# Kernel optimization log

Measured on AMD Instinct MI355X. Metric: run time of the kernel, lower is better.

The kernel has to match this reference:

```python
import jax, jax.numpy as jnp
import numpy as np

# static sizes
B, N_PER, D, H, L, DFF, IN_DIM = 32, 1024, 128, 4, 3, 2048, 64
N = B * N_PER
HD = D // H
EPS = 1e-5


def setup_inputs() -> dict:
    key = jax.random.key(0)
    ks = jax.random.split(key, 16)
    s = 0.02
    rn = lambda k, shp: jax.random.normal(k, shp, jnp.float32) * s
    return {
        "x": jax.random.normal(ks[0], (N, IN_DIM), jnp.float32),
        # uniform graph sizes -> static max_nodes; sorted graph ids
        "batch": jnp.repeat(jnp.arange(B, dtype=jnp.int32), N_PER),
        "W_in": rn(ks[1], (D, IN_DIM)),
        "b_in": rn(ks[2], (D,)),
        "Wqkv": rn(ks[3], (L, 3 * D, D)),
        "bqkv": rn(ks[4], (L, 3 * D)),
        "Wo": rn(ks[5], (L, D, D)),
        "bo": rn(ks[6], (L, D)),
        "W1": rn(ks[7], (L, DFF, D)),
        "b1": rn(ks[8], (L, DFF)),
        "W2": rn(ks[9], (L, D, DFF)),
        "b2": rn(ks[10], (L, D)),
        "ln1_g": jnp.ones((L, D), jnp.float32),
        "ln1_b": jnp.zeros((L, D), jnp.float32),
        "ln2_g": jnp.ones((L, D), jnp.float32),
        "ln2_b": jnp.zeros((L, D), jnp.float32),
    }


def _ln(x, g, b):
    m = x.mean(-1, keepdims=True)
    v = jnp.mean((x - m) ** 2, axis=-1, keepdims=True)
    return (x - m) / jnp.sqrt(v + EPS) * g + b


def _mha(h, Wqkv, bqkv, Wo, bo):
    # h: [B, S, D]
    qkv = h @ Wqkv.T + bqkv                      # [B, S, 3D]
    q, k, v = jnp.split(qkv, 3, axis=-1)
    q = q.reshape(B, -1, H, HD)
    k = k.reshape(B, -1, H, HD)
    v = v.reshape(B, -1, H, HD)
    att = jnp.einsum("bqhd,bkhd->bhqk", q, k) / np.sqrt(HD).astype(np.float32)
    p = jax.nn.softmax(att, axis=-1)
    o = jnp.einsum("bhqk,bkhd->bqhd", p, v).reshape(B, -1, D)
    return o @ Wo.T + bo


def reference(x, batch, W_in, b_in, Wqkv, bqkv, Wo, bo, W1, b1, W2, b2,
              ln1_g, ln1_b, ln2_g, ln2_b):
    # fused ragged -> padded: project all nodes once, scatter by (graph, pos)
    h = x @ W_in.T + b_in                        # [N, D]
    starts = jnp.searchsorted(batch, jnp.arange(B, dtype=batch.dtype))
    pos = jnp.arange(N, dtype=batch.dtype) - starts[batch]
    padded = jnp.zeros((B, N_PER, D), h.dtype).at[batch, pos].set(h)

    out = padded
    for l in range(L):  # post-LN TransformerEncoderLayer, dropout=eval
        a = _mha(out, Wqkv[l], bqkv[l], Wo[l], bo[l])
        out = _ln(out + a, ln1_g[l], ln1_b[l])
        f = jax.nn.relu(out @ W1[l].T + b1[l]) @ W2[l].T + b2[l]
        out = _ln(out + f, ln2_g[l], ln2_b[l])

    # mask derived from projected inputs, exactly as the original
    mask = (padded.sum(axis=2) != 0).astype(out.dtype)  # [B, S]
    return (out * mask[:, :, None]).sum(axis=1) / mask.sum(axis=1, keepdims=True)
```

## Files before the change

kernel.cpp:

```cpp
#include <hip/hip_runtime.h>
#include <hip/hip_bf16.h>
#include <stdint.h>

#define BB    32
#define NPER  1024
#define NTOT  32768
#define DD    128
#define HH    4
#define HD    32
#define LL    3
#define DFF   2048
#define INDIM 64
#define QKSCALE 0.17677669529663687f

typedef unsigned short u16;
typedef short bf16x8 __attribute__((ext_vector_type(8)));
typedef float f32x4 __attribute__((ext_vector_type(4)));

#define AS_GLOBAL(p) ((const __attribute__((address_space(1))) void*)(p))
#define AS_LDS(p)    ((__attribute__((address_space(3))) void*)(p))

__device__ __forceinline__ float bf2f(u16 v){
  unsigned u = ((unsigned)v) << 16; float f; __builtin_memcpy(&f, &u, 4); return f;
}
__device__ __forceinline__ u16 f2bf(float f){
  unsigned u; __builtin_memcpy(&u, &f, 4);
  unsigned lsb = (u >> 16) & 1u;
  u += 0x7fffu + lsb;
  return (u16)(u >> 16);
}

constexpr size_t OFF_FLAG   = 0;
constexpr size_t OFF_STARTS = 256;
constexpr size_t OFF_BIN    = 1024;
constexpr size_t OFF_BQKV   = OFF_BIN   + 128*4;
constexpr size_t OFF_BO     = OFF_BQKV  + 1152*4;
constexpr size_t OFF_B1     = OFF_BO    + 384*4;
constexpr size_t OFF_B2     = OFF_B1    + 6144*4;
constexpr size_t OFF_LN1G   = OFF_B2    + 384*4;
constexpr size_t OFF_LN1B   = OFF_LN1G  + 384*4;
constexpr size_t OFF_LN2G   = OFF_LN1B  + 384*4;
constexpr size_t OFF_LN2B   = OFF_LN2G  + 384*4;
constexpr size_t OFF_XB     = 40960;
constexpr size_t OFF_WINB   = OFF_XB    + (size_t)2097152*2;
constexpr size_t OFF_WQKVB  = OFF_WINB  + (size_t)8192*2;
constexpr size_t OFF_WOB    = OFF_WQKVB + (size_t)147456*2;
constexpr size_t OFF_W1B    = OFF_WOB   + (size_t)49152*2;
constexpr size_t OFF_W2B    = OFF_W1B   + (size_t)786432*2;
constexpr size_t OFF_CUR    = OFF_W2B   + (size_t)786432*2;
constexpr size_t OFF_TMP    = OFF_CUR   + (size_t)4194304*4;
constexpr size_t OFF_CURB   = OFF_TMP   + (size_t)4194304*4;
constexpr size_t OFF_QKVB   = OFF_CURB  + (size_t)4194304*2;
constexpr size_t OFF_ATTNOB = OFF_QKVB  + (size_t)12582912*2;
constexpr size_t OFF_ACTB   = OFF_ATTNOB+ (size_t)4194304*2;
constexpr size_t OFF_MASK   = OFF_ACTB  + (size_t)16777216*2;
constexpr size_t OFF_VT     = OFF_MASK  + (size_t)NTOT*4;
constexpr size_t OFF_RED    = OFF_VT    + (size_t)4096*1024*2;
constexpr size_t OFF_CNT    = OFF_RED   + (size_t)32*8*128*4;

__device__ __forceinline__ int plaus(unsigned bits){
  if ((bits << 1) == 0u) return 1;
  unsigned e = (bits >> 23) & 0xFFu;
  return (e >= 100u && e <= 140u) ? 1 : 0;
}
__global__ void prep_kernel(const unsigned* __restrict__ x, const int* __restrict__ batch,
                            int* __restrict__ flag, int* __restrict__ starts){
  __shared__ int red[256];
  int t = threadIdx.x, c = 0;
  for (int i = t; i < 2048; i += 256){
    unsigned w = x[i];
    c += (plaus(w << 16) & plaus(w & 0xFFFF0000u));
  }
  red[t] = c; __syncthreads();
  for (int s = 128; s > 0; s >>= 1){ if (t < s) red[t] += red[t+s]; __syncthreads(); }
  if (t == 0) *flag = (red[0] >= 1229) ? 1 : 0;
  if (t < BB){
    int lo = 0, hi = NTOT;
    while (lo < hi){ int mid = (lo + hi) >> 1; if (batch[mid] < t) lo = mid + 1; else hi = mid; }
    starts[t] = lo;
  }
}

struct ConvSeg { const void* src; void* dst; int n; int tobf; };
struct ConvArgs { ConvSeg s[14]; };

__global__ __launch_bounds__(256) void convall_kernel(ConvArgs a, const int* __restrict__ flag){
  const int isb = *flag;
  const int blk = blockIdx.x;
  int seg = -1, base = 0, lb = 0;
  #pragma unroll
  for (int i = 0; i < 14; ++i){
    int nb = (a.s[i].n + 1023) >> 10;
    if (seg < 0){
      if (blk < base + nb){ seg = i; lb = blk - base; }
      base += nb;
    }
  }
  const ConvSeg sg = a.s[seg];
  const int idx = lb*1024 + threadIdx.x*4;
  if (idx >= sg.n) return;
  if (sg.tobf){
    u16* dst = (u16*)sg.dst + idx;
    if (isb){
      *(uint2*)dst = *(const uint2*)((const u16*)sg.src + idx);
    } else {
      const float* s4 = (const float*)sg.src + idx;
      dst[0] = f2bf(s4[0]); dst[1] = f2bf(s4[1]);
      dst[2] = f2bf(s4[2]); dst[3] = f2bf(s4[3]);
    }
  } else {
    float* dst = (float*)sg.dst + idx;
    if (isb){
      const u16* s4 = (const u16*)sg.src + idx;
      dst[0] = bf2f(s4[0]); dst[1] = bf2f(s4[1]);
      dst[2] = bf2f(s4[2]); dst[3] = bf2f(s4[3]);
    } else {
      *(float4*)dst = *(const float4*)((const float*)sg.src + idx);
    }
  }
}

__global__ __launch_bounds__(256) void inproj_kernel(
    const void* __restrict__ xraw,
    const u16* __restrict__ WINB,
    const float* __restrict__ bin,
    const int* __restrict__ batch, const int* __restrict__ starts,
    const int* __restrict__ flag,
    float* __restrict__ cur, u16* __restrict__ curb, float* __restrict__ mask)
{
  __shared__ __align__(16) u16 Wl[8192];
  const int t = threadIdx.x, wave = t >> 6, lane = t & 63;
  const int quad = lane >> 4, l16 = lane & 15;
  const int m0 = blockIdx.x * 64;
  const int isb = *flag;

  #pragma unroll
  for (int j = 0; j < 4; ++j){
    int s = t + 256*j;
    int r = s >> 3, c8 = (s & 7) ^ (r & 7);
    *(uint4*)&Wl[s*8] = *(const uint4*)(WINB + (size_t)r*INDIM + c8*8);
  }
  bf16x8 af[2];
  const int arow = m0 + wave*16 + l16;
  if (isb){
    const u16* XB = (const u16*)xraw;
    #pragma unroll
    for (int kk = 0; kk < 2; ++kk)
      af[kk] = *(const bf16x8*)(XB + (size_t)arow*INDIM + kk*32 + quad*8);
  } else {
    const float* Xf = (const float*)xraw;
    #pragma unroll
    for (int kk = 0; kk < 2; ++kk){
      float4 a = *(const float4*)(Xf + (size_t)arow*INDIM + kk*32 + quad*8);
      float4 b = *(const float4*)(Xf + (size_t)arow*INDIM + kk*32 + quad*8 + 4);
      af[kk][0] = (short)f2bf(a.x); af[kk][1] = (short)f2bf(a.y);
      af[kk][2] = (short)f2bf(a.z); af[kk][3] = (short)f2bf(a.w);
      af[kk][4] = (short)f2bf(b.x); af[kk][5] = (short)f2bf(b.y);
      af[kk][6] = (short)f2bf(b.z); af[kk][7] = (short)f2bf(b.w);
    }
  }
  __syncthreads();

  f32x4 O[8];
  #pragma unroll
  for (int nt = 0; nt < 8; ++nt){ O[nt][0]=0.f; O[nt][1]=0.f; O[nt][2]=0.f; O[nt][3]=0.f; }

  #pragma unroll
  for (int nt = 0; nt < 8; ++nt){
    int row = nt*16 + l16;
    bf16x8 wf[2];
    #pragma unroll
    for (int kk = 0; kk < 2; ++kk)
      wf[kk] = *(const bf16x8*)&Wl[(row*8 + ((kk*4 + quad) ^ (row & 7)))*8];
    #pragma unroll
    for (int kk = 0; kk < 2; ++kk)
      O[nt] = __builtin_amdgcn_mfma_f32_16x16x32_bf16(af[kk], wf[kk], O[nt], 0, 0, 0);
  }

  #pragma unroll
  for (int rr = 0; rr < 4; ++rr){
    int node = m0 + wave*16 + quad*4 + rr;
    int gr = batch[node];
    int p  = node - starts[gr];
    float vs[8], sum = 0.f;
    #pragma unroll
    for (int nt = 0; nt < 8; ++nt){
      float v = O[nt][rr] + bin[nt*16 + l16];
      vs[nt] = v; sum += v;
    }
    sum += __shfl_xor(sum, 1); sum += __shfl_xor(sum, 2);
    sum += __shfl_xor(sum, 4); sum += __shfl_xor(sum, 8);
    if ((unsigned)p < (unsigned)NPER && (unsigned)gr < (unsigned)BB){
      size_t j = (size_t)gr*NPER + p;
      #pragma unroll
      for (int nt = 0; nt < 8; ++nt){
        int col = nt*16 + l16;
        cur[j*DD + col]  = vs[nt];
        curb[j*DD + col] = f2bf(vs[nt]);
      }
      if (l16 == 0) mask[j] = (sum != 0.f) ? 1.f : 0.f;
    }
  }
}

__global__ __launch_bounds__(256) void fattn_kernel(
    const u16* __restrict__ qkvb,
    const u16* __restrict__ vt,
    u16* __restrict__ attnob)
{
  __shared__ __align__(16) u16 Klds[2][2048];
  __shared__ __align__(16) u16 Vl[2][2048];
  __shared__ __align__(16) u16 Pl[4][2][16*72];

  const int t = threadIdx.x;
  const int wave = t >> 6, lane = t & 63;
  const int quad = lane >> 4, l16 = lane & 15;
  const int q0 = blockIdx.x * 128;
  const int h = blockIdx.y, b = blockIdx.z;
  const size_t qkvbase = (size_t)b * NPER * 384;
  const u16* Kg = qkvb + qkvbase + 128 + h*HD;
  const u16* Vg = vt + (size_t)((b*HH + h)*HD) * NPER;

  bf16x8 qf[2];
  #pragma unroll
  for (int qt = 0; qt < 2; ++qt){
    const u16* qp = qkvb + qkvbase + (size_t)(q0 + wave*32 + qt*16 + l16)*384 + h*HD + quad*8;
    uint4 qv = *(const uint4*)qp;
    u16 raw[8]; __builtin_memcpy(raw, &qv, 16);
    #pragma unroll
    for (int j = 0; j < 8; ++j) qf[qt][j] = (short)f2bf(bf2f(raw[j]) * QKSCALE);
  }

  const int vcv = wave*2 + (lane >> 5), vd = lane & 31;
  auto stage = [&](int buf, int kt){
    __builtin_amdgcn_global_load_lds(
        AS_GLOBAL(Kg + (size_t)(kt*64 + lane)*384 + wave*8),
        AS_LDS(&Klds[buf][wave*64*8]), 16, 0, 0);
    __builtin_amdgcn_global_load_lds(
        AS_GLOBAL(Vg + (size_t)vd*NPER + kt*64 + vcv*8),
        AS_LDS(&Vl[buf][wave*64*8]), 16, 0, 0);
  };

  float lsum[2] = {0.f, 0.f};
  f32x4 o[2][2];
  #pragma unroll
  for (int qt = 0; qt < 2; ++qt)
    #pragma unroll
    for (int i = 0; i < 2; ++i){ o[qt][i][0]=0.f; o[qt][i][1]=0.f; o[qt][i][2]=0.f; o[qt][i][3]=0.f; }

  stage(0, 0);
  asm volatile("s_waitcnt vmcnt(0)" ::: "memory");
  __syncthreads();

  for (int kt = 0; kt < 16; ++kt){
    const int buf = kt & 1;
    if (kt + 1 < 16) stage(buf ^ 1, kt + 1);

    f32x4 sfr[2][4];
    #pragma unroll
    for (int nt = 0; nt < 4; ++nt){
      bf16x8 kf = *(const bf16x8*)&Klds[buf][(quad*64 + nt*16 + l16)*8];
      f32x4 z = {0.f,0.f,0.f,0.f};
      sfr[0][nt] = __builtin_amdgcn_mfma_f32_16x16x32_bf16(kf, qf[0], z, 0, 0, 0);
      sfr[1][nt] = __builtin_amdgcn_mfma_f32_16x16x32_bf16(kf, qf[1], z, 0, 0, 0);
    }

    #pragma unroll
    for (int qt = 0; qt < 2; ++qt){
      float ps = 0.f;
      #pragma unroll
      for (int nt = 0; nt < 4; ++nt){
        float e0 = __expf(sfr[qt][nt][0]), e1 = __expf(sfr[qt][nt][1]);
        float e2 = __expf(sfr[qt][nt][2]), e3 = __expf(sfr[qt][nt][3]);
        ps += (e0 + e1) + (e2 + e3);
        uint2 w;
        w.x = (unsigned)f2bf(e0) | ((unsigned)f2bf(e1) << 16);
        w.y = (unsigned)f2bf(e2) | ((unsigned)f2bf(e3) << 16);
        *(uint2*)&Pl[wave][qt][l16*72 + nt*16 + quad*4] = w;
      }
      ps += __shfl_xor(ps, 16);
      ps += __shfl_xor(ps, 32);
      lsum[qt] += ps;
    }
    asm volatile("s_waitcnt lgkmcnt(0)" ::: "memory");

    #pragma unroll
    for (int kk = 0; kk < 2; ++kk){
      bf16x8 v0 = *(const bf16x8*)&Vl[buf][((kk*4 + quad)*32 + l16)*8];
      bf16x8 v1 = *(const bf16x8*)&Vl[buf][((kk*4 + quad)*32 + 16 + l16)*8];
      #pragma unroll
      for (int qt = 0; qt < 2; ++qt){
        bf16x8 pf = *(const bf16x8*)&Pl[wave][qt][l16*72 + kk*32 + quad*8];
        o[qt][0] = __builtin_amdgcn_mfma_f32_16x16x32_bf16(pf, v0, o[qt][0], 0, 0, 0);
        o[qt][1] = __builtin_amdgcn_mfma_f32_16x16x32_bf16(pf, v1, o[qt][1], 0, 0, 0);
      }
    }

    if (kt + 1 < 16){
      asm volatile("s_waitcnt vmcnt(0)" ::: "memory");
      __syncthreads();
    }
  }

  #pragma unroll
  for (int qt = 0; qt < 2; ++qt){
    #pragma unroll
    for (int r = 0; r < 4; ++r){
      float inv = 1.f / __shfl(lsum[qt], quad*4 + r);
      int row = q0 + wave*32 + qt*16 + quad*4 + r;
      size_t base = (size_t)(b*NPER + row)*DD + h*HD;
      attnob[base + l16]      = f2bf(o[qt][0][r] * inv);
      attnob[base + 16 + l16] = f2bf(o[qt][1][r] * inv);
    }
  }
}

__device__ __forceinline__ void epilogue_ln64(
    const f32x4 O[8], int m0, int wave, int quad, int l16,
    const float* __restrict__ bias, const float* __restrict__ g,
    const float* __restrict__ beta, float* __restrict__ cur,
    u16* __restrict__ curb)
{
  #pragma unroll
  for (int rr = 0; rr < 4; ++rr){
    int row = m0 + wave*16 + quad*4 + rr;
    float vs[8], sum = 0.f;
    #pragma unroll
    for (int nt = 0; nt < 8; ++nt){
      int col = nt*16 + l16;
      float v = O[nt][rr] + bias[col] + cur[(size_t)row*DD + col];
      vs[nt] = v; sum += v;
    }
    sum += __shfl_xor(sum, 1); sum += __shfl_xor(sum, 2);
    sum += __shfl_xor(sum, 4); sum += __shfl_xor(sum, 8);
    float mean = sum * (1.f/DD);
    float sq = 0.f;
    #pragma unroll
    for (int nt = 0; nt < 8; ++nt){ float d = vs[nt] - mean; sq += d*d; }
    sq += __shfl_xor(sq, 1); sq += __shfl_xor(sq, 2);
    sq += __shfl_xor(sq, 4); sq += __shfl_xor(sq, 8);
    float rs = rsqrtf(sq * (1.f/DD) + 1e-5f);
    #pragma unroll
    for (int nt = 0; nt < 8; ++nt){
      int col = nt*16 + l16;
      float o = (vs[nt] - mean)*rs*g[col] + beta[col];
      cur[(size_t)row*DD + col]  = o;
      curb[(size_t)row*DD + col] = f2bf(o);
    }
  }
}

__global__ __launch_bounds__(256) void wgemm_kernel(
    const u16* __restrict__ A,
    const u16* __restrict__ Wbase,
    const float* __restrict__ biasb,
    float* __restrict__ cur, u16* __restrict__ curb,
    const float* __restrict__ g, const float* __restrict__ beta)
{
  __shared__ __align__(16) u16 Wl[16384];
  const int t = threadIdx.x, wave = t >> 6, lane = t & 63;
  const int quad = lane >> 4, l16 = lane & 15;
  const int m0 = blockIdx.x * 64;

  #pragma unroll
  for (int j = 0; j < 8; ++j){
    int s = t + 256*j;
    int r = s >> 4, cx = (s & 15) ^ (r & 15);
    *(uint4*)&Wl[s*8] = *(const uint4*)(Wbase + (size_t)r*128 + cx*8);
  }
  bf16x8 af[4];
  #pragma unroll
  for (int kk = 0; kk < 4; ++kk)
    af[kk] = *(const bf16x8*)(A + (size_t)(m0 + wave*16 + l16)*128 + kk*32 + quad*8);
  __syncthreads();

  f32x4 O[8];
  #pragma unroll
  for (int nt = 0; nt < 8; ++nt){ O[nt][0]=0.f; O[nt][1]=0.f; O[nt][2]=0.f; O[nt][3]=0.f; }

  #pragma unroll
  for (int nt = 0; nt < 8; ++nt){
    int row = nt*16 + l16;
    bf16x8 wf[4];
    #pragma unroll
    for (int kk = 0; kk < 4; ++kk)
      wf[kk] = *(const bf16x8*)&Wl[(row*16 + ((kk*4 + quad) ^ l16))*8];
    #pragma unroll
    for (int kk = 0; kk < 4; ++kk)
      O[nt] = __builtin_amdgcn_mfma_f32_16x16x32_bf16(af[kk], wf[kk], O[nt], 0, 0, 0);
  }

  epilogue_ln64(O, m0, wave, quad, l16, biasb, g, beta, cur, curb);
}

__global__ __launch_bounds__(256) void wgemm2_kernel(
    const u16* __restrict__ A,
    const u16* __restrict__ Wbase,
    const float* __restrict__ biasb,
    u16* __restrict__ outb, int opitch,
    u16* __restrict__ vtout)
{
  __shared__ __align__(16) u16 Wl[16384];
  const int t = threadIdx.x, wave = t >> 6, lane = t & 63;
  const int quad = lane >> 4, l16 = lane & 15;
  const int m0 = blockIdx.x * 128, nb = blockIdx.y;
  const u16* Wsl = Wbase + (size_t)nb * 16384;
  const float* bias = biasb + nb * 128;

  #pragma unroll
  for (int j = 0; j < 8; ++j){
    int s = t + 256*j;
    int r = s >> 4, cx = (s & 15) ^ (r & 15);
    *(uint4*)&Wl[s*8] = *(const uint4*)(Wsl + (size_t)r*128 + cx*8);
  }
  bf16x8 af[2][4];
  #pragma unroll
  for (int mt = 0; mt < 2; ++mt)
    #pragma unroll
    for (int kk = 0; kk < 4; ++kk)
      af[mt][kk] = *(const bf16x8*)(A + (size_t)(m0 + wave*32 + mt*16 + l16)*128 + kk*32 + quad*8);
  __syncthreads();

  f32x4 O[2][8];
  #pragma unroll
  for (int mt = 0; mt < 2; ++mt)
    #pragma unroll
    for (int nt = 0; nt < 8; ++nt){ O[mt][nt][0]=0.f; O[mt][nt][1]=0.f; O[mt][nt][2]=0.f; O[mt][nt][3]=0.f; }

  #pragma unroll
  for (int nt = 0; nt < 8; ++nt){
    int row = nt*16 + l16;
    bf16x8 wf[4];
    #pragma unroll
    for (int kk = 0; kk < 4; ++kk)
      wf[kk] = *(const bf16x8*)&Wl[(row*16 + ((kk*4 + quad) ^ l16))*8];
    #pragma unroll
    for (int mt = 0; mt < 2; ++mt)
      #pragma unroll
      for (int kk = 0; kk < 4; ++kk)
        O[mt][nt] = __builtin_amdgcn_mfma_f32_16x16x32_bf16(af[mt][kk], wf[kk], O[mt][nt], 0, 0, 0);
  }

  if (nb == 2){
    #pragma unroll
    for (int mt = 0; mt < 2; ++mt){
      int rowb = m0 + wave*32 + mt*16 + quad*4;
      int bg = rowb >> 10, s = rowb & 1023;
      #pragma unroll
      for (int nt = 0; nt < 8; ++nt){
        int col = nt*16 + l16;
        int hh = col >> 5, d = col & 31;
        float v0 = O[mt][nt][0] + bias[col], v1 = O[mt][nt][1] + bias[col];
        float v2 = O[mt][nt][2] + bias[col], v3 = O[mt][nt][3] + bias[col];
        uint2 w;
        w.x = (unsigned)f2bf(v0) | ((unsigned)f2bf(v1) << 16);
        w.y = (unsigned)f2bf(v2) | ((unsigned)f2bf(v3) << 16);
        *(uint2*)(vtout + (size_t)((bg*HH + hh)*HD + d)*NPER + s) = w;
      }
    }
  } else {
    #pragma unroll
    for (int mt = 0; mt < 2; ++mt)
      #pragma unroll
      for (int rr = 0; rr < 4; ++rr){
        int row = m0 + wave*32 + mt*16 + quad*4 + rr;
        #pragma unroll
        for (int nt = 0; nt < 8; ++nt){
          int col = nt*16 + l16;
          outb[(size_t)row*opitch + nb*128 + col] = f2bf(O[mt][nt][rr] + bias[col]);
        }
      }
  }
}

__global__ __launch_bounds__(256, 2) void ffn_kernel(
    const u16* __restrict__ Ag,
    const u16* __restrict__ W1g,
    const u16* __restrict__ W2g,
    const float* __restrict__ b1,
    const float* __restrict__ b2,
    const float* __restrict__ g, const float* __restrict__ beta,
    float* __restrict__ cur, u16* __restrict__ curb)
{
  __shared__ __align__(16) u16 W1l[2][8192];
  __shared__ __align__(16) u16 W2l[2][8192];
  __shared__ __align__(16) u16 Pl[4][16*72];

  const int t = threadIdx.x, wave = t >> 6, lane = t & 63;
  const int quad = lane >> 4, l16 = lane & 15;
  const int m0 = blockIdx.x * 64;
  u16* Pw = &Pl[wave][0];

  auto stage = [&](int buf, int dffc){
    #pragma unroll
    for (int i = 0; i < 4; ++i){
      const int s0 = wave*256 + i*64;
      const int s  = s0 + lane;
      { int r = s >> 4, cx = (s & 15) ^ (r & 15);
        __builtin_amdgcn_global_load_lds(
            AS_GLOBAL(W1g + (size_t)(dffc + r)*128 + cx*8),
            AS_LDS(&W1l[buf][s0*8]), 16, 0, 0); }
      { int r = s >> 3, cx = (s & 7) ^ (r & 7);
        __builtin_amdgcn_global_load_lds(
            AS_GLOBAL(W2g + (size_t)r*DFF + dffc + cx*8),
            AS_LDS(&W2l[buf][s0*8]), 16, 0, 0); }
    }
  };

  bf16x8 af[4];
  #pragma unroll
  for (int kk = 0; kk < 4; ++kk)
    af[kk] = *(const bf16x8*)(Ag + (size_t)(m0 + wave*16 + l16)*128 + kk*32 + quad*8);

  f32x4 O[8];
  #pragma unroll
  for (int nt = 0; nt < 8; ++nt){ O[nt][0]=0.f; O[nt][1]=0.f; O[nt][2]=0.f; O[nt][3]=0.f; }

  stage(0, 0);
  asm volatile("s_waitcnt vmcnt(0)" ::: "memory");
  __syncthreads();

  for (int c = 0; c < 32; ++c){
    const int buf = c & 1;
    if (c + 1 < 32) stage(buf ^ 1, (c + 1)*64);

    #pragma unroll
    for (int nt = 0; nt < 4; ++nt){
      int row = nt*16 + l16;
      bf16x8 wf[4];
      #pragma unroll
      for (int kk = 0; kk < 4; ++kk)
        wf[kk] = *(const bf16x8*)&W1l[buf][(row*16 + ((kk*4 + quad) ^ l16))*8];
      float b1v = b1[c*64 + row];
      f32x4 s = {0.f,0.f,0.f,0.f};
      #pragma unroll
      for (int kk = 0; kk < 4; ++kk)
        s = __builtin_amdgcn_mfma_f32_16x16x32_bf16(af[kk], wf[kk], s, 0, 0, 0);
      #pragma unroll
      for (int rr = 0; rr < 4; ++rr)
        Pw[(quad*4 + rr)*72 + nt*16 + l16] = f2bf(fmaxf(s[rr] + b1v, 0.f));
    }
    asm volatile("s_waitcnt lgkmcnt(0)" ::: "memory");

    bf16x8 pf[2];
    #pragma unroll
    for (int kk = 0; kk < 2; ++kk)
      pf[kk] = *(const bf16x8*)&Pw[l16*72 + kk*32 + quad*8];
    #pragma unroll
    for (int nt = 0; nt < 8; ++nt){
      int row = nt*16 + l16;
      bf16x8 wf[2];
      #pragma unroll
      for (int kk = 0; kk < 2; ++kk)
        wf[kk] = *(const bf16x8*)&W2l[buf][(row*8 + ((kk*4 + quad) ^ (l16 & 7)))*8];
      #pragma unroll
      for (int kk = 0; kk < 2; ++kk)
        O[nt] = __builtin_amdgcn_mfma_f32_16x16x32_bf16(pf[kk], wf[kk], O[nt], 0, 0, 0);
    }

    if (c + 1 < 32){
      asm volatile("s_waitcnt vmcnt(0)" ::: "memory");
      __syncthreads();
    }
  }

  epilogue_ln64(O, m0, wave, quad, l16, b2, g, beta, cur, curb);
}

__global__ __launch_bounds__(128) void reduce1_kernel(
    const float* __restrict__ cur, const float* __restrict__ mask,
    float* __restrict__ partial, float* __restrict__ cnt)
{
  int b = blockIdx.x, c = blockIdx.y, t = threadIdx.x;
  float acc = 0.f, cn = 0.f;
  for (int s = c*128; s < c*128 + 128; ++s){
    float mk = mask[b*NPER + s];
    acc += cur[(size_t)(b*NPER + s)*DD + t] * mk;
    cn += mk;
  }
  partial[(size_t)(b*8 + c)*DD + t] = acc;
  if (t == 0) cnt[b*8 + c] = cn;
}
__global__ __launch_bounds__(128) void reduce2_kernel(
    const float* __restrict__ partial, const float* __restrict__ cnt,
    const int* __restrict__ flag, void* __restrict__ out)
{
  int b = blockIdx.x, t = threadIdx.x;
  float acc = 0.f, cn = 0.f;
  #pragma unroll
  for (int c = 0; c < 8; ++c){
    acc += partial[(size_t)(b*8 + c)*DD + t];
    cn  += cnt[b*8 + c];
  }
  float val = acc / cn;
  if (*flag) ((u16*)out)[b*DD + t] = f2bf(val);
  else       ((float*)out)[b*DD + t] = val;
}

extern "C" void kernel_launch(void* const* d_in, const int* in_sizes, int n_in,
                              void* d_out, int out_size, void* d_ws, size_t ws_size,
                              hipStream_t stream)
{
  (void)in_sizes; (void)n_in; (void)out_size; (void)ws_size;
  char* ws = (char*)d_ws;
  int*   flag   = (int*)(ws + OFF_FLAG);
  int*   starts = (int*)(ws + OFF_STARTS);
  float* BIN  = (float*)(ws + OFF_BIN);
  float* BQKV = (float*)(ws + OFF_BQKV);
  float* BO   = (float*)(ws + OFF_BO);
  float* B1   = (float*)(ws + OFF_B1);
  float* B2   = (float*)(ws + OFF_B2);
  float* LN1G = (float*)(ws + OFF_LN1G);
  float* LN1B = (float*)(ws + OFF_LN1B);
  float* LN2G = (float*)(ws + OFF_LN2G);
  float* LN2B = (float*)(ws + OFF_LN2B);
  u16* WINB  = (u16*)(ws + OFF_WINB);
  u16* WQKVB = (u16*)(ws + OFF_WQKVB);
  u16* WOB   = (u16*)(ws + OFF_WOB);
  u16* W1B   = (u16*)(ws + OFF_W1B);
  u16* W2B   = (u16*)(ws + OFF_W2B);
  float* CUR = (float*)(ws + OFF_CUR);
  u16* CURB  = (u16*)(ws + OFF_CURB);
  u16* QKVB  = (u16*)(ws + OFF_QKVB);
  u16* ATTNOB= (u16*)(ws + OFF_ATTNOB);
  float* MASK= (float*)(ws + OFF_MASK);
  u16* VT    = (u16*)(ws + OFF_VT);
  float* RED = (float*)(ws + OFF_RED);
  float* CNT = (float*)(ws + OFF_CNT);

  prep_kernel<<<1, 256, 0, stream>>>((const unsigned*)d_in[0], (const int*)d_in[1],
                                     flag, starts);

  ConvArgs ca;
  ca.s[0]  = { d_in[2],  WINB,  DD*INDIM,   1 };
  ca.s[1]  = { d_in[4],  WQKVB, LL*3*DD*DD, 1 };
  ca.s[2]  = { d_in[6],  WOB,   LL*DD*DD,   1 };
  ca.s[3]  = { d_in[8],  W1B,   LL*DFF*DD,  1 };
  ca.s[4]  = { d_in[10], W2B,   LL*DD*DFF,  1 };
  ca.s[5]  = { d_in[3],  BIN,   DD,         0 };
  ca.s[6]  = { d_in[5],  BQKV,  LL*3*DD,    0 };
  ca.s[7]  = { d_in[7],  BO,    LL*DD,      0 };
  ca.s[8]  = { d_in[9],  B1,    LL*DFF,     0 };
  ca.s[9]  = { d_in[11], B2,    LL*DD,      0 };
  ca.s[10] = { d_in[12], LN1G,  LL*DD,      0 };
  ca.s[11] = { d_in[13], LN1B,  LL*DD,      0 };
  ca.s[12] = { d_in[14], LN2G,  LL*DD,      0 };
  ca.s[13] = { d_in[15], LN2B,  LL*DD,      0 };
  int nblk = 0;
  for (int i = 0; i < 14; ++i) nblk += (ca.s[i].n + 1023) >> 10;
  convall_kernel<<<nblk, 256, 0, stream>>>(ca, flag);

  inproj_kernel<<<NTOT/64, 256, 0, stream>>>(
      d_in[0], WINB, BIN, (const int*)d_in[1], starts, flag, CUR, CURB, MASK);

  for (int l = 0; l < LL; ++l){
    wgemm2_kernel<<<dim3(NTOT/128, 3), 256, 0, stream>>>(
        CURB, WQKVB + (size_t)l*3*DD*DD, BQKV + l*3*DD, QKVB, 384, VT);
    fattn_kernel<<<dim3(NPER/128, HH, BB), 256, 0, stream>>>(QKVB, VT, ATTNOB);
    wgemm_kernel<<<dim3(NTOT/64), 256, 0, stream>>>(
        ATTNOB, WOB + (size_t)l*DD*DD, BO + l*DD, CUR, CURB, LN1G + l*DD, LN1B + l*DD);
    ffn_kernel<<<dim3(NTOT/64), 256, 0, stream>>>(
        CURB, W1B + (size_t)l*DFF*DD, W2B + (size_t)l*DD*DFF,
        B1 + l*DFF, B2 + l*DD, LN2G + l*DD, LN2B + l*DD, CUR, CURB);
  }

  reduce1_kernel<<<dim3(BB, 8), 128, 0, stream>>>(CUR, MASK, RED, CNT);
  reduce2_kernel<<<BB, 128, 0, stream>>>(RED, CNT, flag, d_out);
}
```

Measured before the change: 488.1 us.

## Fuse attention output projection and first LayerNorm into the FFN kernel

Removes the separate Wo GEMM + LayerNorm kernel and performs it at the start of the FFN kernel for the same 64-row tile. The normalized result stays in registers as the FFN residual and is passed to the W1 GEMM via shared memory, avoiding a global write/read of the fp32 and bf16 activations and one launch per layer. The cost is more live registers across the FFN loop and an extra Wo load per block, which could cause spills or reduce occupancy.

```diff
diff --git a/kernel.cpp b/kernel.cpp
--- a/kernel.cpp
+++ b/kernel.cpp
@@ -315,84 +315,6 @@
   }
 }
 
-__device__ __forceinline__ void epilogue_ln64(
-    const f32x4 O[8], int m0, int wave, int quad, int l16,
-    const float* __restrict__ bias, const float* __restrict__ g,
-    const float* __restrict__ beta, float* __restrict__ cur,
-    u16* __restrict__ curb)
-{
-  #pragma unroll
-  for (int rr = 0; rr < 4; ++rr){
-    int row = m0 + wave*16 + quad*4 + rr;
-    float vs[8], sum = 0.f;
-    #pragma unroll
-    for (int nt = 0; nt < 8; ++nt){
-      int col = nt*16 + l16;
-      float v = O[nt][rr] + bias[col] + cur[(size_t)row*DD + col];
-      vs[nt] = v; sum += v;
-    }
-    sum += __shfl_xor(sum, 1); sum += __shfl_xor(sum, 2);
-    sum += __shfl_xor(sum, 4); sum += __shfl_xor(sum, 8);
-    float mean = sum * (1.f/DD);
-    float sq = 0.f;
-    #pragma unroll
-    for (int nt = 0; nt < 8; ++nt){ float d = vs[nt] - mean; sq += d*d; }
-    sq += __shfl_xor(sq, 1); sq += __shfl_xor(sq, 2);
-    sq += __shfl_xor(sq, 4); sq += __shfl_xor(sq, 8);
-    float rs = rsqrtf(sq * (1.f/DD) + 1e-5f);
-    #pragma unroll
-    for (int nt = 0; nt < 8; ++nt){
-      int col = nt*16 + l16;
-      float o = (vs[nt] - mean)*rs*g[col] + beta[col];
-      cur[(size_t)row*DD + col]  = o;
-      curb[(size_t)row*DD + col] = f2bf(o);
-    }
-  }
-}
-
-__global__ __launch_bounds__(256) void wgemm_kernel(
-    const u16* __restrict__ A,
-    const u16* __restrict__ Wbase,
-    const float* __restrict__ biasb,
-    float* __restrict__ cur, u16* __restrict__ curb,
-    const float* __restrict__ g, const float* __restrict__ beta)
-{
-  __shared__ __align__(16) u16 Wl[16384];
-  const int t = threadIdx.x, wave = t >> 6, lane = t & 63;
-  const int quad = lane >> 4, l16 = lane & 15;
-  const int m0 = blockIdx.x * 64;
-
-  #pragma unroll
-  for (int j = 0; j < 8; ++j){
-    int s = t + 256*j;
-    int r = s >> 4, cx = (s & 15) ^ (r & 15);
-    *(uint4*)&Wl[s*8] = *(const uint4*)(Wbase + (size_t)r*128 + cx*8);
-  }
-  bf16x8 af[4];
-  #pragma unroll
-  for (int kk = 0; kk < 4; ++kk)
-    af[kk] = *(const bf16x8*)(A + (size_t)(m0 + wave*16 + l16)*128 + kk*32 + quad*8);
-  __syncthreads();
-
-  f32x4 O[8];
-  #pragma unroll
-  for (int nt = 0; nt < 8; ++nt){ O[nt][0]=0.f; O[nt][1]=0.f; O[nt][2]=0.f; O[nt][3]=0.f; }
-
-  #pragma unroll
-  for (int nt = 0; nt < 8; ++nt){
-    int row = nt*16 + l16;
-    bf16x8 wf[4];
-    #pragma unroll
-    for (int kk = 0; kk < 4; ++kk)
-      wf[kk] = *(const bf16x8*)&Wl[(row*16 + ((kk*4 + quad) ^ l16))*8];
-    #pragma unroll
-    for (int kk = 0; kk < 4; ++kk)
-      O[nt] = __builtin_amdgcn_mfma_f32_16x16x32_bf16(af[kk], wf[kk], O[nt], 0, 0, 0);
-  }
-
-  epilogue_ln64(O, m0, wave, quad, l16, biasb, g, beta, cur, curb);
-}
-
 __global__ __launch_bounds__(256) void wgemm2_kernel(
     const u16* __restrict__ A,
     const u16* __restrict__ Wbase,
@@ -474,22 +396,90 @@
 }
 
 __global__ __launch_bounds__(256, 2) void ffn_kernel(
-    const u16* __restrict__ Ag,
+    const u16* __restrict__ attnob,
+    const u16* __restrict__ Wog,
+    const float* __restrict__ bo,
+    const float* __restrict__ g1, const float* __restrict__ beta1,
     const u16* __restrict__ W1g,
     const u16* __restrict__ W2g,
     const float* __restrict__ b1,
     const float* __restrict__ b2,
-    const float* __restrict__ g, const float* __restrict__ beta,
+    const float* __restrict__ g2, const float* __restrict__ beta2,
     float* __restrict__ cur, u16* __restrict__ curb)
 {
-  __shared__ __align__(16) u16 W1l[2][8192];
-  __shared__ __align__(16) u16 W2l[2][8192];
-  __shared__ __align__(16) u16 Pl[4][16*72];
-
+  __shared__ __align__(16) u16 SM[37376];
   const int t = threadIdx.x, wave = t >> 6, lane = t & 63;
   const int quad = lane >> 4, l16 = lane & 15;
   const int m0 = blockIdx.x * 64;
-  u16* Pw = &Pl[wave][0];
+  u16* Pw = &SM[32768 + wave*1152];
+
+  #pragma unroll
+  for (int i = 0; i < 8; ++i){
+    int s0 = wave*512 + i*64;
+    int s = s0 + lane;
+    int r = s >> 4, cx = (s & 15) ^ (r & 15);
+    __builtin_amdgcn_global_load_lds(
+        AS_GLOBAL(Wog + (size_t)r*128 + cx*8),
+        AS_LDS(&SM[16384 + s0*8]), 16, 0, 0);
+  }
+  bf16x8 afo[4];
+  #pragma unroll
+  for (int kk = 0; kk < 4; ++kk)
+    afo[kk] = *(const bf16x8*)(attnob + (size_t)(m0 + wave*16 + l16)*128 + kk*32 + quad*8);
+  asm volatile("s_waitcnt vmcnt(0)" ::: "memory");
+  __syncthreads();
+
+  f32x4 O[8];
+  #pragma unroll
+  for (int nt = 0; nt < 8; ++nt){ O[nt][0]=0.f; O[nt][1]=0.f; O[nt][2]=0.f; O[nt][3]=0.f; }
+  #pragma unroll
+  for (int nt = 0; nt < 8; ++nt){
+    int row = nt*16 + l16;
+    bf16x8 wf[4];
+    #pragma unroll
+    for (int kk = 0; kk < 4; ++kk)
+      wf[kk] = *(const bf16x8*)&SM[16384 + (row*16 + ((kk*4 + quad) ^ l16))*8];
+    #pragma unroll
+    for (int kk = 0; kk < 4; ++kk)
+      O[nt] = __builtin_amdgcn_mfma_f32_16x16x32_bf16(afo[kk], wf[kk], O[nt], 0, 0, 0);
+  }
+
+  float res[8][4];
+  u16* Tw = &SM[wave*2176];
+  #pragma unroll
+  for (int rr = 0; rr < 4; ++rr){
+    int row = m0 + wave*16 + quad*4 + rr;
+    float vs[8], sum = 0.f;
+    #pragma unroll
+    for (int nt = 0; nt < 8; ++nt){
+      int col = nt*16 + l16;
+      float v = O[nt][rr] + bo[col] + cur[(size_t)row*DD + col];
+      vs[nt] = v; sum += v;
+    }
+    sum += __shfl_xor(sum, 1); sum += __shfl_xor(sum, 2);
+    sum += __shfl_xor(sum, 4); sum += __shfl_xor(sum, 8);
+    float mean = sum * (1.f/DD);
+    float sq = 0.f;
+    #pragma unroll
+    for (int nt = 0; nt < 8; ++nt){ float d = vs[nt] - mean; sq += d*d; }
+    sq += __shfl_xor(sq, 1); sq += __shfl_xor(sq, 2);
+    sq += __shfl_xor(sq, 4); sq += __shfl_xor(sq, 8);
+    float rs = rsqrtf(sq * (1.f/DD) + 1e-5f);
+    #pragma unroll
+    for (int nt = 0; nt < 8; ++nt){
+      int col = nt*16 + l16;
+      float o = (vs[nt] - mean)*rs*g1[col] + beta1[col];
+      res[nt][rr] = o;
+      Tw[(quad*4 + rr)*136 + col] = f2bf(o);
+    }
+  }
+  asm volatile("s_waitcnt lgkmcnt(0)" ::: "memory");
+
+  bf16x8 af[4];
+  #pragma unroll
+  for (int kk = 0; kk < 4; ++kk)
+    af[kk] = *(const bf16x8*)&Tw[l16*136 + kk*32 + quad*8];
+  __syncthreads();
 
   auto stage = [&](int buf, int dffc){
     #pragma unroll
@@ -499,20 +489,14 @@
       { int r = s >> 4, cx = (s & 15) ^ (r & 15);
         __builtin_amdgcn_global_load_lds(
             AS_GLOBAL(W1g + (size_t)(dffc + r)*128 + cx*8),
-            AS_LDS(&W1l[buf][s0*8]), 16, 0, 0); }
+            AS_LDS(&SM[buf*8192 + s0*8]), 16, 0, 0); }
       { int r = s >> 3, cx = (s & 7) ^ (r & 7);
         __builtin_amdgcn_global_load_lds(
             AS_GLOBAL(W2g + (size_t)r*DFF + dffc + cx*8),
-            AS_LDS(&W2l[buf][s0*8]), 16, 0, 0); }
+            AS_LDS(&SM[16384 + buf*8192 + s0*8]), 16, 0, 0); }
     }
   };
 
-  bf16x8 af[4];
-  #pragma unroll
-  for (int kk = 0; kk < 4; ++kk)
-    af[kk] = *(const bf16x8*)(Ag + (size_t)(m0 + wave*16 + l16)*128 + kk*32 + quad*8);
-
-  f32x4 O[8];
   #pragma unroll
   for (int nt = 0; nt < 8; ++nt){ O[nt][0]=0.f; O[nt][1]=0.f; O[nt][2]=0.f; O[nt][3]=0.f; }
 
@@ -530,7 +514,7 @@
       bf16x8 wf[4];
       #pragma unroll
       for (int kk = 0; kk < 4; ++kk)
-        wf[kk] = *(const bf16x8*)&W1l[buf][(row*16 + ((kk*4 + quad) ^ l16))*8];
+        wf[kk] = *(const bf16x8*)&SM[buf*8192 + (row*16 + ((kk*4 + quad) ^ l16))*8];
       float b1v = b1[c*64 + row];
       f32x4 s = {0.f,0.f,0.f,0.f};
       #pragma unroll
@@ -552,7 +536,7 @@
       bf16x8 wf[2];
       #pragma unroll
       for (int kk = 0; kk < 2; ++kk)
-        wf[kk] = *(const bf16x8*)&W2l[buf][(row*8 + ((kk*4 + quad) ^ (l16 & 7)))*8];
+        wf[kk] = *(const bf16x8*)&SM[16384 + buf*8192 + (row*8 + ((kk*4 + quad) ^ (l16 & 7)))*8];
       #pragma unroll
       for (int kk = 0; kk < 2; ++kk)
         O[nt] = __builtin_amdgcn_mfma_f32_16x16x32_bf16(pf[kk], wf[kk], O[nt], 0, 0, 0);
@@ -564,7 +548,33 @@
     }
   }
 
-  epilogue_ln64(O, m0, wave, quad, l16, b2, g, beta, cur, curb);
+  #pragma unroll
+  for (int rr = 0; rr < 4; ++rr){
+    int row = m0 + wave*16 + quad*4 + rr;
+    float vs[8], sum = 0.f;
+    #pragma unroll
+    for (int nt = 0; nt < 8; ++nt){
+      int col = nt*16 + l16;
+      float v = O[nt][rr] + b2[col] + res[nt][rr];
+      vs[nt] = v; sum += v;
+    }
+    sum += __shfl_xor(sum, 1); sum += __shfl_xor(sum, 2);
+    sum += __shfl_xor(sum, 4); sum += __shfl_xor(sum, 8);
+    float mean = sum * (1.f/DD);
+    float sq = 0.f;
+    #pragma unroll
+    for (int nt = 0; nt < 8; ++nt){ float d = vs[nt] - mean; sq += d*d; }
+    sq += __shfl_xor(sq, 1); sq += __shfl_xor(sq, 2);
+    sq += __shfl_xor(sq, 4); sq += __shfl_xor(sq, 8);
+    float rs = rsqrtf(sq * (1.f/DD) + 1e-5f);
+    #pragma unroll
+    for (int nt = 0; nt < 8; ++nt){
+      int col = nt*16 + l16;
+      float o = (vs[nt] - mean)*rs*g2[col] + beta2[col];
+      cur[(size_t)row*DD + col]  = o;
+      curb[(size_t)row*DD + col] = f2bf(o);
+    }
+  }
 }
 
 __global__ __launch_bounds__(128) void reduce1_kernel(
@@ -657,10 +667,9 @@
     wgemm2_kernel<<<dim3(NTOT/128, 3), 256, 0, stream>>>(
         CURB, WQKVB + (size_t)l*3*DD*DD, BQKV + l*3*DD, QKVB, 384, VT);
     fattn_kernel<<<dim3(NPER/128, HH, BB), 256, 0, stream>>>(QKVB, VT, ATTNOB);
-    wgemm_kernel<<<dim3(NTOT/64), 256, 0, stream>>>(
-        ATTNOB, WOB + (size_t)l*DD*DD, BO + l*DD, CUR, CURB, LN1G + l*DD, LN1B + l*DD);
     ffn_kernel<<<dim3(NTOT/64), 256, 0, stream>>>(
-        CURB, W1B + (size_t)l*DFF*DD, W2B + (size_t)l*DD*DFF,
+        ATTNOB, WOB + (size_t)l*DD*DD, BO + l*DD, LN1G + l*DD, LN1B + l*DD,
+        W1B + (size_t)l*DFF*DD, W2B + (size_t)l*DD*DFF,
         B1 + l*DFF, B2 + l*DD, LN2G + l*DD, LN2B + l*DD, CUR, CURB);
   }
 
```

Result: no change. 479.5 us (-1.8%).
